# Kernel tuning notes

Hardware: AMD Instinct MI355X
Metric: run time of the kernel (lower is better)

The kernel has to match this reference:

```python
import jax, jax.numpy as jnp
import numpy as np

B, CIN, COUT, H, W = 16, 64, 64, 256, 256
M1, M2 = 32, 32


def setup_inputs() -> dict:
    key = jax.random.key(0)
    k = jax.random.split(key, 7)
    x = jax.random.normal(k[0], (B, CIN, H, W), dtype=jnp.float32)
    # emulate int8 quantized weights: stored values in [-128, 127]
    q_weights1 = jax.random.randint(k[1], (CIN, COUT, M1, M2, 2), -128, 128, dtype=jnp.int32)
    q_weights2 = jax.random.randint(k[2], (CIN, COUT, M1, M2, 2), -128, 128, dtype=jnp.int32)
    w1_scale = jax.random.uniform(k[3], (1,), dtype=jnp.float32) * 0.01 + 0.001
    w1_min = jax.random.normal(k[4], (1,), dtype=jnp.float32) * 0.1
    w2_scale = jax.random.uniform(k[5], (1,), dtype=jnp.float32) * 0.01 + 0.001
    w2_min = jax.random.normal(k[6], (1,), dtype=jnp.float32) * 0.1
    return {"x": x, "q_weights1": q_weights1, "q_weights2": q_weights2,
            "w1_scale": w1_scale, "w1_min": w1_min,
            "w2_scale": w2_scale, "w2_min": w2_min}


def _dequant_complex(q, scale, min_val):
    # (q + 127) * scale + min, then view last dim (re, im) as complex
    w = (q.astype(jnp.float32) + 127.0) * scale + min_val
    return jax.lax.complex(w[..., 0], w[..., 1])


def reference(x, q_weights1, q_weights2, w1_scale, w1_min, w2_scale, w2_min):
    b, cin, h, w = x.shape
    # rfft2 with ortho norm, complex64
    x_ft = jnp.fft.rfft2(x, norm="ortho")  # [B, Cin, H, W//2+1]

    w1c = _dequant_complex(q_weights1, w1_scale[0], w1_min[0])  # [Cin, Cout, M1, M2]
    w2c = _dequant_complex(q_weights2, w2_scale[0], w2_min[0])

    # complex multiply + channel contraction on the retained low/high modes
    out1 = jnp.einsum("bixy,ioxy->boxy", x_ft[:, :, :M1, :M2], w1c)
    out2 = jnp.einsum("bixy,ioxy->boxy", x_ft[:, :, h - M1:, :M2], w2c)

    out_ft = jnp.zeros((b, COUT, h, w // 2 + 1), dtype=x_ft.dtype)
    out_ft = out_ft.at[:, :, :M1, :M2].set(out1)
    out_ft = out_ft.at[:, :, h - M1:, :M2].set(out2)

    return jnp.fft.irfft2(out_ft, s=(h, w), norm="ortho")  # [B, Cout, H, W] float32
```

## Files before the change

kernel.cpp:

```cpp
#include <hip/hip_runtime.h>
#include <math.h>

#define NB 16
#define NCIN 64
#define NCOUT 64
#define NH 256
#define NW 256
#define NM 64
#define NKX 32
#define INV256 (1.0f/256.0f)

typedef __attribute__((ext_vector_type(8))) short short8v;
typedef __attribute__((ext_vector_type(4))) float f32x4;
typedef unsigned short u16;
typedef unsigned int u32;

__device__ __forceinline__ void bf16_split(float v, u16& hi, u16& lo) {
    u32 b = __float_as_uint(v);
    u32 hib = b & 0xffff0000u;
    float lof = v - __uint_as_float(hib);
    hi = (u16)(hib >> 16);
    lo = (u16)(__float_as_uint(lof) >> 16);
}

__device__ __forceinline__ u16 bf16_rtn(float v) {
    u32 b = __float_as_uint(v);
    u32 r = b + 0x7fffu + ((b >> 16) & 1u);
    return (u16)(r >> 16);
}

__global__ __launch_bounds__(256) void init_tw(u16* __restrict__ tw) {
    const int tid = blockIdx.x * 256 + threadIdx.x;
    const float TWO_PI = 6.28318530717958647692f;
    if (tid < 16384) {
        const int e = tid & 7, lane = (tid >> 3) & 63;
        const int nt = (tid >> 9) & 3, kc = tid >> 11;
        const int w = kc * 32 + (lane >> 4) * 8 + e;
        const int n = nt * 16 + (lane & 15);
        const int kx = n >> 1, p = n & 1;
        const float ang = TWO_PI * (float)((kx * w) & 255) * INV256;
        const float v = p ? -sinf(ang) : cosf(ang);
        u16 hi, lo; bf16_split(v, hi, lo);
        tw[tid] = hi; tw[16384 + tid] = lo;
    } else {
        const int u = tid - 16384;
        const int e = u & 7, lane = (u >> 3) & 63;
        const int kc = (u >> 9) & 7, mt = u >> 12;
        const int m = mt * 16 + (lane & 15);
        const int h = kc * 32 + (lane >> 4) * 8 + e;
        const int ky = (m < 32) ? m : (192 + m);
        const float ang = TWO_PI * (float)((ky * h) & 255) * INV256;
        const float c = cosf(ang), s = sinf(ang);
        u16 hi, lo;
        bf16_split(c,  hi, lo); tw[32768 + u] = hi; tw[49152 + u]  = lo;
        bf16_split(s,  hi, lo); tw[65536 + u] = hi; tw[81920 + u]  = lo;
        bf16_split(-s, hi, lo); tw[98304 + u] = hi; tw[114688 + u] = lo;
    }
}

__global__ __launch_bounds__(256) void init_tw2(u16* __restrict__ tw2) {
    const int tid = blockIdx.x * 256 + threadIdx.x;
    const float TWO_PI = 6.28318530717958647692f;
    if (tid < 16384) {
        const int e = tid & 7, lane = (tid >> 3) & 63;
        const int kc = (tid >> 9) & 1, HT = tid >> 10;
        const int h = HT * 16 + (lane & 15);
        const int m = kc * 32 + ((lane >> 4) << 3) + e;
        const int ky = (m < 32) ? m : (192 + m);
        const float ang = TWO_PI * (float)((ky * h) & 255) * INV256;
        tw2[tid]         = bf16_rtn(cosf(ang));
        tw2[16384 + tid] = bf16_rtn(sinf(ang));
        tw2[32768 + tid] = bf16_rtn(-sinf(ang));
    } else {
        const int u = tid - 16384;
        const int e = u & 7, lane = (u >> 3) & 63;
        const int kc = (u >> 9) & 1, nt = u >> 10;
        const int w = nt * 16 + (lane & 15);
        const int kk = kc * 32 + ((lane >> 4) << 3) + e;
        const int kx = kk >> 1, c = kk & 1;
        const float wt = (kx == 0) ? 1.f : 2.f;
        const float ang = TWO_PI * (float)((kx * w) & 255) * INV256;
        const float v = c ? (-wt * sinf(ang) * INV256) : (wt * cosf(ang) * INV256);
        tw2[49152 + u] = bf16_rtn(v);
    }
}

__global__ __launch_bounds__(256) void fwd_mfma(const float* __restrict__ x,
                                                const u16* __restrict__ tw,
                                                float2* __restrict__ xft) {
    __shared__ u16 planes[4 * 32 * 264];
    const int t = threadIdx.x;
    const int lane = t & 63;
    const int wv = t >> 6;
    const int l15 = lane & 15;
    const int lk = lane >> 4;
    const float* __restrict__ xb = x + (size_t)blockIdx.x * (NH * NW);

    const u16* __restrict__ T1h = tw;
    const u16* __restrict__ T1l = tw + 16384;

    for (int mt = 0; mt < 4; ++mt) {
        const int hbase = wv * 64 + mt * 16;
        f32x4 acc[4] = {f32x4{0,0,0,0}, f32x4{0,0,0,0}, f32x4{0,0,0,0}, f32x4{0,0,0,0}};
        for (int kc = 0; kc < 8; ++kc) {
            const float* xr = xb + (size_t)(hbase + l15) * NW + kc * 32 + lk * 8;
            const float4 xa = *(const float4*)xr;
            const float4 xc = *(const float4*)(xr + 4);
            const float v[8] = {xa.x, xa.y, xa.z, xa.w, xc.x, xc.y, xc.z, xc.w};
            short8v Ah, Al;
            #pragma unroll
            for (int e = 0; e < 8; ++e) {
                u16 hi, lo; bf16_split(v[e], hi, lo);
                Ah[e] = (short)hi; Al[e] = (short)lo;
            }
            const int tbase = (kc * 4) * 512 + lane * 8;
            #pragma unroll
            for (int nt = 0; nt < 4; ++nt) {
                const short8v Bh = *(const short8v*)(T1h + tbase + nt * 512);
                const short8v Bl = *(const short8v*)(T1l + tbase + nt * 512);
                acc[nt] = __builtin_amdgcn_mfma_f32_16x16x32_bf16(Ah, Bh, acc[nt], 0, 0, 0);
                acc[nt] = __builtin_amdgcn_mfma_f32_16x16x32_bf16(Ah, Bl, acc[nt], 0, 0, 0);
                acc[nt] = __builtin_amdgcn_mfma_f32_16x16x32_bf16(Al, Bh, acc[nt], 0, 0, 0);
            }
        }
        #pragma unroll
        for (int nt = 0; nt < 4; ++nt) {
            const int n = nt * 16 + l15;
            const int kx = n >> 1, p = n & 1;
            #pragma unroll
            for (int r = 0; r < 4; ++r) {
                const int h = hbase + lk * 4 + r;
                u16 hi, lo; bf16_split(acc[nt][r], hi, lo);
                planes[(2 * p) * 8448 + kx * 264 + h] = hi;
                planes[(2 * p + 1) * 8448 + kx * 264 + h] = lo;
            }
        }
    }
    __syncthreads();

    const u16* __restrict__ C2h = tw + 32768;
    const u16* __restrict__ C2l = tw + 49152;
    const u16* __restrict__ S2h = tw + 65536;
    const u16* __restrict__ S2l = tw + 81920;
    const u16* __restrict__ Snh = tw + 98304;
    const u16* __restrict__ Snl = tw + 114688;

    f32x4 zre[2] = {f32x4{0,0,0,0}, f32x4{0,0,0,0}};
    f32x4 zim[2] = {f32x4{0,0,0,0}, f32x4{0,0,0,0}};
    for (int kc = 0; kc < 8; ++kc) {
        const int abase = (wv * 8 + kc) * 512 + lane * 8;
        const short8v Ch = *(const short8v*)(C2h + abase);
        const short8v Cl = *(const short8v*)(C2l + abase);
        const short8v Sh = *(const short8v*)(S2h + abase);
        const short8v Sl = *(const short8v*)(S2l + abase);
        const short8v Nh = *(const short8v*)(Snh + abase);
        const short8v Nl = *(const short8v*)(Snl + abase);
        #pragma unroll
        for (int nt = 0; nt < 2; ++nt) {
            const int kx = nt * 16 + l15;
            const int off = kx * 264 + kc * 32 + lk * 8;
            const short8v Yrh = *(const short8v*)(planes + off);
            const short8v Yrl = *(const short8v*)(planes + 8448 + off);
            const short8v Yih = *(const short8v*)(planes + 16896 + off);
            const short8v Yil = *(const short8v*)(planes + 25344 + off);
            zre[nt] = __builtin_amdgcn_mfma_f32_16x16x32_bf16(Ch, Yrh, zre[nt], 0, 0, 0);
            zre[nt] = __builtin_amdgcn_mfma_f32_16x16x32_bf16(Ch, Yrl, zre[nt], 0, 0, 0);
            zre[nt] = __builtin_amdgcn_mfma_f32_16x16x32_bf16(Cl, Yrh, zre[nt], 0, 0, 0);
            zre[nt] = __builtin_amdgcn_mfma_f32_16x16x32_bf16(Sh, Yih, zre[nt], 0, 0, 0);
            zre[nt] = __builtin_amdgcn_mfma_f32_16x16x32_bf16(Sh, Yil, zre[nt], 0, 0, 0);
            zre[nt] = __builtin_amdgcn_mfma_f32_16x16x32_bf16(Sl, Yih, zre[nt], 0, 0, 0);
            zim[nt] = __builtin_amdgcn_mfma_f32_16x16x32_bf16(Ch, Yih, zim[nt], 0, 0, 0);
            zim[nt] = __builtin_amdgcn_mfma_f32_16x16x32_bf16(Ch, Yil, zim[nt], 0, 0, 0);
            zim[nt] = __builtin_amdgcn_mfma_f32_16x16x32_bf16(Cl, Yih, zim[nt], 0, 0, 0);
            zim[nt] = __builtin_amdgcn_mfma_f32_16x16x32_bf16(Nh, Yrh, zim[nt], 0, 0, 0);
            zim[nt] = __builtin_amdgcn_mfma_f32_16x16x32_bf16(Nh, Yrl, zim[nt], 0, 0, 0);
            zim[nt] = __builtin_amdgcn_mfma_f32_16x16x32_bf16(Nl, Yrh, zim[nt], 0, 0, 0);
        }
    }
    float2* __restrict__ op = xft + (size_t)blockIdx.x * (NM * NKX);
    #pragma unroll
    for (int nt = 0; nt < 2; ++nt) {
        const int kx = nt * 16 + l15;
        #pragma unroll
        for (int r = 0; r < 4; ++r) {
            const int m = wv * 16 + lk * 4 + r;
            op[m * NKX + kx] = make_float2(zre[nt][r] * INV256, zim[nt][r] * INV256);
        }
    }
}

__global__ __launch_bounds__(256) void mode_v3(const float2* __restrict__ xft,
                                               const int* __restrict__ q1,
                                               const int* __restrict__ q2,
                                               const float* __restrict__ w1s,
                                               const float* __restrict__ w1m,
                                               const float* __restrict__ w2s,
                                               const float* __restrict__ w2m,
                                               float2* __restrict__ oft) {
    __shared__ float2 xs[2][16][8];
    __shared__ float2 ws[2][16][9];
    const int m  = blockIdx.x;
    const int og = blockIdx.y;
    const int kh = blockIdx.z;
    const int t = threadIdx.x;
    const int b = t >> 4, o = t & 15;
    const int mm = (m < 32) ? m : (m - 32);
    const int2* __restrict__ qp = (const int2*)((m < 32) ? q1 : q2);
    const float scale = (m < 32) ? w1s[0] : w2s[0];
    const float wmin  = (m < 32) ? w1m[0] : w2m[0];

    const bool isx = t < 128;
    const int r8 = (t & 127) >> 3;
    const int k8 = t & 7;

    const float2* __restrict__ xsrc = xft + (size_t)(r8 * 64) * (NM * NKX)
                                          + m * NKX + kh * 8 + k8;
    const int2* __restrict__ wsrc = qp + (size_t)(og * 16 + r8) * 1024
                                       + mm * 32 + kh * 8 + k8;

    float2 pxa, pxb; int2 pwa, pwb;
    if (isx) {
        const float2 p0 = xsrc[0];
        xs[0][r8][k8] = p0;
        pxb = xsrc[(size_t)1 * (NM * NKX)];
        pxa = xsrc[(size_t)2 * (NM * NKX)];
    } else {
        const int2 p0 = wsrc[0];
        ws[0][r8][k8] = make_float2(((float)p0.x + 127.0f) * scale + wmin,
                                    ((float)p0.y + 127.0f) * scale + wmin);
        pwb = wsrc[(size_t)1 * 65536];
        pwa = wsrc[(size_t)2 * 65536];
    }
    __syncthreads();

    float accr[8], acci[8];
    #pragma unroll
    for (int k = 0; k < 8; ++k) { accr[k] = 0.f; acci[k] = 0.f; }

    #pragma unroll 1
    for (int j = 0; j < 32; ++j) {
        const int i0 = 2 * j;
        #pragma unroll
        for (int k = 0; k < 8; ++k) {
            const float2 xv = xs[0][b][k];
            const float2 wv = ws[0][o][k];
            accr[k] += xv.x * wv.x - xv.y * wv.y;
            acci[k] += xv.x * wv.y + xv.y * wv.x;
        }
        {
            if (isx) xs[1][r8][k8] = pxb;
            else     ws[1][r8][k8] = make_float2(((float)pwb.x + 127.0f) * scale + wmin,
                                                 ((float)pwb.y + 127.0f) * scale + wmin);
            __syncthreads();
            if (i0 + 3 < 64) {
                if (isx) pxb = xsrc[(size_t)(i0 + 3) * (NM * NKX)];
                else     pwb = wsrc[(size_t)(i0 + 3) * 65536];
            }
        }
        const int i1 = 2 * j + 1;
        #pragma unroll
        for (int k = 0; k < 8; ++k) {
            const float2 xv = xs[1][b][k];
            const float2 wv = ws[1][o][k];
            accr[k] += xv.x * wv.x - xv.y * wv.y;
            acci[k] += xv.x * wv.y + xv.y * wv.x;
        }
        if (i1 < 63) {
            if (isx) xs[0][r8][k8] = pxa;
            else     ws[0][r8][k8] = make_float2(((float)pwa.x + 127.0f) * scale + wmin,
                                                 ((float)pwa.y + 127.0f) * scale + wmin);
            __syncthreads();
            if (i1 + 3 < 64) {
                if (isx) pxa = xsrc[(size_t)(i1 + 3) * (NM * NKX)];
                else     pwa = wsrc[(size_t)(i1 + 3) * 65536];
            }
        }
    }

    float2* __restrict__ op = oft + ((size_t)(b * 64 + og * 16 + o) * NM + m) * NKX + kh * 8;
    #pragma unroll
    for (int k = 0; k < 8; ++k) op[k] = make_float2(accr[k], acci[k]);
}

__global__ __launch_bounds__(256) void inv_mfma(const float2* __restrict__ oft,
                                                const u16* __restrict__ tw2,
                                                float* __restrict__ out) {
    __shared__ u16 lds[13824];
    const int t = threadIdx.x;
    const int lane = t & 63;
    const int wv = t >> 6;
    const int l15 = lane & 15;
    const int lk = lane >> 4;
    const int hh = blockIdx.y;

    const float2* __restrict__ ip = oft + (size_t)blockIdx.x * (NM * NKX);
    #pragma unroll
    for (int r = 0; r < 8; ++r) {
        const int idx = r * 256 + t;
        const int m = idx >> 5, kx = idx & 31;
        const float2 v = ip[idx];
        lds[kx * 72 + m]        = bf16_rtn(v.x);
        lds[2304 + kx * 72 + m] = bf16_rtn(v.y);
    }
    __syncthreads();

    const u16* __restrict__ C4 = tw2;
    const u16* __restrict__ S4 = tw2 + 16384;
    const u16* __restrict__ N4 = tw2 + 32768;

    short8v Br[2][2], Bi[2][2];
    #pragma unroll
    for (int nt = 0; nt < 2; ++nt) {
        #pragma unroll
        for (int kc = 0; kc < 2; ++kc) {
            const int off = (nt * 16 + l15) * 72 + kc * 32 + lk * 8;
            Br[nt][kc] = *(const short8v*)(lds + off);
            Bi[nt][kc] = *(const short8v*)(lds + 2304 + off);
        }
    }

    #pragma unroll
    for (int mt = 0; mt < 2; ++mt) {
        const int lt = wv * 2 + mt;
        const int HT = hh * 8 + lt;
        f32x4 zr[2] = {f32x4{0,0,0,0}, f32x4{0,0,0,0}};
        f32x4 zi[2] = {f32x4{0,0,0,0}, f32x4{0,0,0,0}};
        #pragma unroll
        for (int kc = 0; kc < 2; ++kc) {
            const int abase = ((HT * 2 + kc) * 64 + lane) * 8;
            const short8v C = *(const short8v*)(C4 + abase);
            const short8v S = *(const short8v*)(S4 + abase);
            const short8v N = *(const short8v*)(N4 + abase);
            #pragma unroll
            for (int nt = 0; nt < 2; ++nt) {
                zr[nt] = __builtin_amdgcn_mfma_f32_16x16x32_bf16(C, Br[nt][kc], zr[nt], 0, 0, 0);
                zr[nt] = __builtin_amdgcn_mfma_f32_16x16x32_bf16(N, Bi[nt][kc], zr[nt], 0, 0, 0);
                zi[nt] = __builtin_amdgcn_mfma_f32_16x16x32_bf16(S, Br[nt][kc], zi[nt], 0, 0, 0);
                zi[nt] = __builtin_amdgcn_mfma_f32_16x16x32_bf16(C, Bi[nt][kc], zi[nt], 0, 0, 0);
            }
        }
        #pragma unroll
        for (int nt = 0; nt < 2; ++nt) {
            const int kx = nt * 16 + l15;
            #pragma unroll
            for (int r = 0; r < 4; ++r) {
                const int hl = lt * 16 + lk * 4 + r;
                const u32 pk = (u32)bf16_rtn(zr[nt][r]) | ((u32)bf16_rtn(zi[nt][r]) << 16);
                *(u32*)(lds + 4608 + hl * 72 + 2 * kx) = pk;
            }
        }
    }
    __syncthreads();

    const u16* __restrict__ W5 = tw2 + 49152;
    float* __restrict__ op = out + (size_t)blockIdx.x * (NH * NW) + hh * 128 * NW;
    for (int nt = 0; nt < 16; ++nt) {
        const short8v B0 = *(const short8v*)(W5 + ((nt * 2 + 0) * 64 + lane) * 8);
        const short8v B1 = *(const short8v*)(W5 + ((nt * 2 + 1) * 64 + lane) * 8);
        const int w = nt * 16 + l15;
        #pragma unroll
        for (int mt = 0; mt < 2; ++mt) {
            const int lt = wv * 2 + mt;
            const int h0 = lt * 16 + l15;
            const short8v A0 = *(const short8v*)(lds + 4608 + h0 * 72 + lk * 8);
            const short8v A1 = *(const short8v*)(lds + 4608 + h0 * 72 + 32 + lk * 8);
            f32x4 acc = {0, 0, 0, 0};
            acc = __builtin_amdgcn_mfma_f32_16x16x32_bf16(A0, B0, acc, 0, 0, 0);
            acc = __builtin_amdgcn_mfma_f32_16x16x32_bf16(A1, B1, acc, 0, 0, 0);
            #pragma unroll
            for (int r = 0; r < 4; ++r) {
                const int hl = lt * 16 + lk * 4 + r;
                op[hl * 256 + w] = acc[r];
            }
        }
    }
}

extern "C" void kernel_launch(void* const* d_in, const int* in_sizes, int n_in,
                              void* d_out, int out_size, void* d_ws, size_t ws_size,
                              hipStream_t stream) {
    const float* x  = (const float*)d_in[0];
    const int* q1   = (const int*)d_in[1];
    const int* q2   = (const int*)d_in[2];
    const float* w1s = (const float*)d_in[3];
    const float* w1m = (const float*)d_in[4];
    const float* w2s = (const float*)d_in[5];
    const float* w2m = (const float*)d_in[6];
    float* out = (float*)d_out;

    float2* xft = (float2*)d_ws;
    float2* oft = xft + (size_t)NB * NCIN * NM * NKX;
    u16* tw  = (u16*)oft;
    u16* tw2 = (u16*)xft;

    init_tw<<<128, 256, 0, stream>>>(tw);
    fwd_mfma<<<NB * NCIN, 256, 0, stream>>>(x, tw, xft);
    mode_v3<<<dim3(NM, 4, 4), 256, 0, stream>>>(xft, q1, q2, w1s, w1m, w2s, w2m, oft);
    init_tw2<<<128, 256, 0, stream>>>(tw2);
    inv_mfma<<<dim3(NB * NCOUT, 2), 256, 0, stream>>>(oft, tw2, out);
}
```

Baseline: 220.4 us.

## Split mode contraction over input-channel halves, vectorize loads, reorder inverse MFMA

New measurement: 252.3 us. 1.14x slower.

```diff
diff --git a/kernel.cpp b/kernel.cpp
--- a/kernel.cpp
+++ b/kernel.cpp
@@ -189,47 +189,53 @@
     }
 }
 
-__global__ __launch_bounds__(256) void mode_v3(const float2* __restrict__ xft,
+__global__ __launch_bounds__(256) void mode_v4(const float2* __restrict__ xft,
                                                const int* __restrict__ q1,
                                                const int* __restrict__ q2,
                                                const float* __restrict__ w1s,
                                                const float* __restrict__ w1m,
                                                const float* __restrict__ w2s,
                                                const float* __restrict__ w2m,
-                                               float2* __restrict__ oft) {
-    __shared__ float2 xs[2][16][8];
-    __shared__ float2 ws[2][16][9];
+                                               float2* __restrict__ oft0,
+                                               float2* __restrict__ oft1) {
+    __shared__ float2 xs2[2][16][8];
+    __shared__ float2 ws2[2][8][16];
     const int m  = blockIdx.x;
     const int og = blockIdx.y;
-    const int kh = blockIdx.z;
+    const int kh = blockIdx.z >> 1;
+    const int ih = blockIdx.z & 1;
     const int t = threadIdx.x;
     const int b = t >> 4, o = t & 15;
     const int mm = (m < 32) ? m : (m - 32);
-    const int2* __restrict__ qp = (const int2*)((m < 32) ? q1 : q2);
+    const int* __restrict__ q = (m < 32) ? q1 : q2;
     const float scale = (m < 32) ? w1s[0] : w2s[0];
     const float wmin  = (m < 32) ? w1m[0] : w2m[0];
-
-    const bool isx = t < 128;
-    const int r8 = (t & 127) >> 3;
-    const int k8 = t & 7;
-
-    const float2* __restrict__ xsrc = xft + (size_t)(r8 * 64) * (NM * NKX)
-                                          + m * NKX + kh * 8 + k8;
-    const int2* __restrict__ wsrc = qp + (size_t)(og * 16 + r8) * 1024
-                                       + mm * 32 + kh * 8 + k8;
-
-    float2 pxa, pxb; int2 pwa, pwb;
+    const int ib = ih * 32;
+
+    const bool isx = (t < 64);
+    const bool isw = (t >= 64) && (t < 128);
+    const int lr = (t & 63) >> 2;
+    const int kp = t & 3;
+
+    const float4* __restrict__ xsrc = (const float4*)xft
+        + (size_t)(lr * 64 + ib) * 1024 + m * 16 + kh * 4 + kp;
+    const int4* __restrict__ wsrc = (const int4*)q
+        + ((size_t)ib * 64 + og * 16 + lr) * 512 + mm * 16 + kh * 4 + kp;
+
+    float4 pxa, pxb; int4 pwa, pwb;
     if (isx) {
-        const float2 p0 = xsrc[0];
-        xs[0][r8][k8] = p0;
-        pxb = xsrc[(size_t)1 * (NM * NKX)];
-        pxa = xsrc[(size_t)2 * (NM * NKX)];
-    } else {
-        const int2 p0 = wsrc[0];
-        ws[0][r8][k8] = make_float2(((float)p0.x + 127.0f) * scale + wmin,
-                                    ((float)p0.y + 127.0f) * scale + wmin);
-        pwb = wsrc[(size_t)1 * 65536];
-        pwa = wsrc[(size_t)2 * 65536];
+        const float4 p0 = xsrc[0];
+        *(float4*)&xs2[0][lr][kp * 2] = p0;
+        pxb = xsrc[1024];
+        pxa = xsrc[2048];
+    } else if (isw) {
+        const int4 p0 = wsrc[0];
+        ws2[0][kp * 2][lr]     = make_float2(((float)p0.x + 127.f) * scale + wmin,
+                                             ((float)p0.y + 127.f) * scale + wmin);
+        ws2[0][kp * 2 + 1][lr] = make_float2(((float)p0.z + 127.f) * scale + wmin,
+                                             ((float)p0.w + 127.f) * scale + wmin);
+        pwb = wsrc[32768];
+        pwa = wsrc[65536];
     }
     __syncthreads();
 
@@ -238,53 +244,61 @@
     for (int k = 0; k < 8; ++k) { accr[k] = 0.f; acci[k] = 0.f; }
 
     #pragma unroll 1
-    for (int j = 0; j < 32; ++j) {
-        const int i0 = 2 * j;
+    for (int j = 0; j < 16; ++j) {
         #pragma unroll
         for (int k = 0; k < 8; ++k) {
-            const float2 xv = xs[0][b][k];
-            const float2 wv = ws[0][o][k];
+            const float2 xv = xs2[0][b][k];
+            const float2 wv = ws2[0][k][o];
             accr[k] += xv.x * wv.x - xv.y * wv.y;
             acci[k] += xv.x * wv.y + xv.y * wv.x;
         }
-        {
-            if (isx) xs[1][r8][k8] = pxb;
-            else     ws[1][r8][k8] = make_float2(((float)pwb.x + 127.0f) * scale + wmin,
-                                                 ((float)pwb.y + 127.0f) * scale + wmin);
-            __syncthreads();
-            if (i0 + 3 < 64) {
-                if (isx) pxb = xsrc[(size_t)(i0 + 3) * (NM * NKX)];
-                else     pwb = wsrc[(size_t)(i0 + 3) * 65536];
-            }
-        }
-        const int i1 = 2 * j + 1;
+        if (isx) *(float4*)&xs2[1][lr][kp * 2] = pxb;
+        else if (isw) {
+            ws2[1][kp * 2][lr]     = make_float2(((float)pwb.x + 127.f) * scale + wmin,
+                                                 ((float)pwb.y + 127.f) * scale + wmin);
+            ws2[1][kp * 2 + 1][lr] = make_float2(((float)pwb.z + 127.f) * scale + wmin,
+                                                 ((float)pwb.w + 127.f) * scale + wmin);
+        }
+        __syncthreads();
+        if (2 * j + 3 < 32) {
+            if (isx) pxb = xsrc[(size_t)(2 * j + 3) * 1024];
+            else if (isw) pwb = wsrc[(size_t)(2 * j + 3) * 32768];
+        }
         #pragma unroll
         for (int k = 0; k < 8; ++k) {
-            const float2 xv = xs[1][b][k];
-            const float2 wv = ws[1][o][k];
+            const float2 xv = xs2[1][b][k];
+            const float2 wv = ws2[1][k][o];
             accr[k] += xv.x * wv.x - xv.y * wv.y;
             acci[k] += xv.x * wv.y + xv.y * wv.x;
         }
-        if (i1 < 63) {
-            if (isx) xs[0][r8][k8] = pxa;
-            else     ws[0][r8][k8] = make_float2(((float)pwa.x + 127.0f) * scale + wmin,
-                                                 ((float)pwa.y + 127.0f) * scale + wmin);
+        if (2 * j + 2 < 32) {
+            if (isx) *(float4*)&xs2[0][lr][kp * 2] = pxa;
+            else if (isw) {
+                ws2[0][kp * 2][lr]     = make_float2(((float)pwa.x + 127.f) * scale + wmin,
+                                                     ((float)pwa.y + 127.f) * scale + wmin);
+                ws2[0][kp * 2 + 1][lr] = make_float2(((float)pwa.z + 127.f) * scale + wmin,
+                                                     ((float)pwa.w + 127.f) * scale + wmin);
+            }
             __syncthreads();
-            if (i1 + 3 < 64) {
-                if (isx) pxa = xsrc[(size_t)(i1 + 3) * (NM * NKX)];
-                else     pwa = wsrc[(size_t)(i1 + 3) * 65536];
-            }
-        }
-    }
-
-    float2* __restrict__ op = oft + ((size_t)(b * 64 + og * 16 + o) * NM + m) * NKX + kh * 8;
-    #pragma unroll
-    for (int k = 0; k < 8; ++k) op[k] = make_float2(accr[k], acci[k]);
-}
-
-__global__ __launch_bounds__(256) void inv_mfma(const float2* __restrict__ oft,
-                                                const u16* __restrict__ tw2,
-                                                float* __restrict__ out) {
+            if (2 * j + 4 < 32) {
+                if (isx) pxa = xsrc[(size_t)(2 * j + 4) * 1024];
+                else if (isw) pwa = wsrc[(size_t)(2 * j + 4) * 32768];
+            }
+        }
+    }
+
+    float2* __restrict__ oftP = ih ? oft1 : oft0;
+    float4* __restrict__ op4 = (float4*)(oftP
+        + ((size_t)(b * 64 + og * 16 + o) * NM + m) * NKX + kh * 8);
+    #pragma unroll
+    for (int k2 = 0; k2 < 4; ++k2)
+        op4[k2] = make_float4(accr[2 * k2], acci[2 * k2], accr[2 * k2 + 1], acci[2 * k2 + 1]);
+}
+
+__global__ __launch_bounds__(256) void inv_mfma2(const float2* __restrict__ oft0,
+                                                 const float2* __restrict__ oft1,
+                                                 const u16* __restrict__ tw2,
+                                                 float* __restrict__ out) {
     __shared__ u16 lds[13824];
     const int t = threadIdx.x;
     const int lane = t & 63;
@@ -293,14 +307,19 @@
     const int lk = lane >> 4;
     const int hh = blockIdx.y;
 
-    const float2* __restrict__ ip = oft + (size_t)blockIdx.x * (NM * NKX);
-    #pragma unroll
-    for (int r = 0; r < 8; ++r) {
-        const int idx = r * 256 + t;
-        const int m = idx >> 5, kx = idx & 31;
-        const float2 v = ip[idx];
-        lds[kx * 72 + m]        = bf16_rtn(v.x);
-        lds[2304 + kx * 72 + m] = bf16_rtn(v.y);
+    const float4* __restrict__ p0 = (const float4*)(oft0 + (size_t)blockIdx.x * (NM * NKX));
+    const float4* __restrict__ p1 = (const float4*)(oft1 + (size_t)blockIdx.x * (NM * NKX));
+    #pragma unroll
+    for (int rep = 0; rep < 4; ++rep) {
+        const int idx4 = rep * 256 + t;
+        const float4 a = p0[idx4];
+        const float4 c = p1[idx4];
+        const int e0 = idx4 * 2;
+        const int m = e0 >> 5, kx = e0 & 31;
+        lds[kx * 72 + m]              = bf16_rtn(a.x + c.x);
+        lds[2304 + kx * 72 + m]       = bf16_rtn(a.y + c.y);
+        lds[(kx + 1) * 72 + m]        = bf16_rtn(a.z + c.z);
+        lds[2304 + (kx + 1) * 72 + m] = bf16_rtn(a.w + c.w);
     }
     __syncthreads();
 
@@ -353,25 +372,28 @@
     __syncthreads();
 
     const u16* __restrict__ W5 = tw2 + 49152;
-    float* __restrict__ op = out + (size_t)blockIdx.x * (NH * NW) + hh * 128 * NW;
-    for (int nt = 0; nt < 16; ++nt) {
-        const short8v B0 = *(const short8v*)(W5 + ((nt * 2 + 0) * 64 + lane) * 8);
-        const short8v B1 = *(const short8v*)(W5 + ((nt * 2 + 1) * 64 + lane) * 8);
-        const int w = nt * 16 + l15;
+    float* __restrict__ op = out + (size_t)blockIdx.x * (NH * NW) + (size_t)hh * 128 * NW;
+
+    short8v Bz[2][2];
+    #pragma unroll
+    for (int mt = 0; mt < 2; ++mt) {
+        const int lt = wv * 2 + mt;
+        #pragma unroll
+        for (int kc = 0; kc < 2; ++kc)
+            Bz[mt][kc] = *(const short8v*)(lds + 4608 + (lt * 16 + l15) * 72 + kc * 32 + lk * 8);
+    }
+
+    for (int wt = 0; wt < 16; ++wt) {
+        const short8v A0 = *(const short8v*)(W5 + ((wt * 2 + 0) * 64 + lane) * 8);
+        const short8v A1 = *(const short8v*)(W5 + ((wt * 2 + 1) * 64 + lane) * 8);
         #pragma unroll
         for (int mt = 0; mt < 2; ++mt) {
             const int lt = wv * 2 + mt;
-            const int h0 = lt * 16 + l15;
-            const short8v A0 = *(const short8v*)(lds + 4608 + h0 * 72 + lk * 8);
-            const short8v A1 = *(const short8v*)(lds + 4608 + h0 * 72 + 32 + lk * 8);
             f32x4 acc = {0, 0, 0, 0};
-            acc = __builtin_amdgcn_mfma_f32_16x16x32_bf16(A0, B0, acc, 0, 0, 0);
-            acc = __builtin_amdgcn_mfma_f32_16x16x32_bf16(A1, B1, acc, 0, 0, 0);
-            #pragma unroll
-            for (int r = 0; r < 4; ++r) {
-                const int hl = lt * 16 + lk * 4 + r;
-                op[hl * 256 + w] = acc[r];
-            }
+            acc = __builtin_amdgcn_mfma_f32_16x16x32_bf16(A0, Bz[mt][0], acc, 0, 0, 0);
+            acc = __builtin_amdgcn_mfma_f32_16x16x32_bf16(A1, Bz[mt][1], acc, 0, 0, 0);
+            *(float4*)&op[(lt * 16 + l15) * 256 + wt * 16 + lk * 4] =
+                make_float4(acc[0], acc[1], acc[2], acc[3]);
         }
     }
 }
@@ -388,14 +410,15 @@
     const float* w2m = (const float*)d_in[6];
     float* out = (float*)d_out;
 
-    float2* xft = (float2*)d_ws;
-    float2* oft = xft + (size_t)NB * NCIN * NM * NKX;
-    u16* tw  = (u16*)oft;
-    u16* tw2 = (u16*)xft;
+    float2* xft  = (float2*)d_ws;
+    float2* oft0 = xft + (size_t)NB * NCIN * NM * NKX;
+    float2* oft1 = oft0 + (size_t)NB * NCOUT * NM * NKX;
+    u16* tw  = (u16*)((char*)d_ws + (size_t)48 * 1024 * 1024);
+    u16* tw2 = tw + 131072;
 
     init_tw<<<128, 256, 0, stream>>>(tw);
+    init_tw2<<<128, 256, 0, stream>>>(tw2);
     fwd_mfma<<<NB * NCIN, 256, 0, stream>>>(x, tw, xft);
-    mode_v3<<<dim3(NM, 4, 4), 256, 0, stream>>>(xft, q1, q2, w1s, w1m, w2s, w2m, oft);
-    init_tw2<<<128, 256, 0, stream>>>(tw2);
-    inv_mfma<<<dim3(NB * NCOUT, 2), 256, 0, stream>>>(oft, tw2, out);
-}
+    mode_v4<<<dim3(NM, 4, 8), 256, 0, stream>>>(xft, q1, q2, w1s, w1m, w2s, w2m, oft0, oft1);
+    inv_mfma2<<<dim3(NB * NCOUT, 2), 256, 0, stream>>>(oft0, oft1, tw2, out);
+}
```
